# Kernel optimization log

Measured on AMD Instinct MI355X. Metric: run time of the kernel, lower is better.

## Reference

```python
import jax, jax.numpy as jnp
import numpy as np

N_NODES = 200000
N_EDGES = 6400000
N_GRAPHS = 128


def setup_inputs() -> dict:
    key = jax.random.key(0)
    k1, k2, k3, k4, k5, k6, k7 = jax.random.split(key, 7)
    x = jax.random.normal(k1, (N_NODES, 1), dtype=jnp.float32)
    edge_index = jax.random.randint(k2, (2, N_EDGES), 0, N_NODES, dtype=jnp.int64)
    batch = jnp.sort(jax.random.randint(k3, (N_NODES,), 0, N_GRAPHS, dtype=jnp.int64))
    # GCNConv parameters (glorot-ish scale)
    W1 = jax.random.normal(k4, (1, 32), dtype=jnp.float32) * (1.0 / np.sqrt(1 + 32))
    b1 = jnp.zeros((32,), dtype=jnp.float32)
    W2 = jax.random.normal(k5, (32, 8), dtype=jnp.float32) * (1.0 / np.sqrt(32 + 8))
    b2 = jnp.zeros((8,), dtype=jnp.float32)
    return {"x": x, "edge_index": edge_index, "batch": batch,
            "W1": W1, "b1": b1, "W2": W2, "b2": b2}


def _gcn_conv(x, src, dst, W, b):
    # x: [N, din] -> [N, dout]; PyG GCNConv: symmetric-normalized A+I aggregation
    h = x @ W                                            # [N, dout]
    deg = jax.ops.segment_sum(jnp.ones_like(dst, h.dtype), dst, num_segments=N_NODES)
    dinv = jnp.where(deg > 0, jax.lax.rsqrt(deg), 0.0)    # [N]
    norm = dinv[src] * dinv[dst]                          # [E+N]
    msg = h[src] * norm[:, None]                          # gather + scale
    out = jax.ops.segment_sum(msg, dst, num_segments=N_NODES)
    return out + b


def reference(x, edge_index, batch, W1, b1, W2, b2):
    loop = jnp.arange(N_NODES, dtype=edge_index.dtype)
    src = jnp.concatenate([edge_index[0], loop])          # add self-loops
    dst = jnp.concatenate([edge_index[1], loop])
    h = _gcn_conv(x, src, dst, W1, b1)
    h = _gcn_conv(h, src, dst, W2, b2)
    # global mean pool over graphs
    sums = jax.ops.segment_sum(h, batch, num_segments=N_GRAPHS)
    cnts = jax.ops.segment_sum(jnp.ones((N_NODES,), h.dtype), batch, num_segments=N_GRAPHS)
    pooled = sums / jnp.maximum(cnts, 1.0)[:, None]       # [G, 8]
    return jax.nn.log_softmax(pooled, axis=1)
```

## Files before the change

### kernel.cpp

```cpp
#include <hip/hip_runtime.h>
#include <math.h>

#define N_NODES 200000
#define N_EDGES 6400000
#define N_GRAPHS 128

#define NBK   782
#define EBLK  256
#define EPB   (N_EDGES / EBLK)


__global__ void kA0_hist(const int* __restrict__ dst, unsigned* __restrict__ countMat) {
    __shared__ unsigned cnt[NBK];
    for (int t = threadIdx.x; t < NBK; t += blockDim.x) cnt[t] = 0;
    __syncthreads();
    const int4* d4 = (const int4*)(dst + blockIdx.x * EPB);
    for (int e = threadIdx.x; e < EPB / 4; e += blockDim.x) {
        int4 d = d4[e];
        atomicAdd(&cnt[d.x >> 8], 1u);
        atomicAdd(&cnt[d.y >> 8], 1u);
        atomicAdd(&cnt[d.z >> 8], 1u);
        atomicAdd(&cnt[d.w >> 8], 1u);
    }
    __syncthreads();
    for (int t = threadIdx.x; t < NBK; t += blockDim.x)
        countMat[blockIdx.x * NBK + t] = cnt[t];
}

__global__ void kScanBlk(unsigned* __restrict__ mat, unsigned* __restrict__ colsum) {
    int bkt = blockIdx.x * 4 + (threadIdx.x >> 6);
    if (bkt >= NBK) return;
    int lane = threadIdx.x & 63;
    unsigned carry = 0;
    for (int k = 0; k < 4; ++k) {
        int blk = k * 64 + lane;
        unsigned v = mat[blk * NBK + bkt];
        unsigned s = v;
        for (int off = 1; off < 64; off <<= 1) {
            unsigned u = __shfl_up(s, off);
            if (lane >= off) s += u;
        }
        mat[blk * NBK + bkt] = carry + s - v;
        carry += __shfl(s, 63);
    }
    colsum[bkt] = carry;
}

__global__ void kScanBkt(const unsigned* __restrict__ colsum, unsigned* __restrict__ bucketBase) {
    __shared__ unsigned wsum[16];
    int t = threadIdx.x;
    int lane = t & 63, w = t >> 6;
    unsigned v = (t < NBK) ? colsum[t] : 0u;
    unsigned s = v;
    for (int off = 1; off < 64; off <<= 1) {
        unsigned u = __shfl_up(s, off);
        if (lane >= off) s += u;
    }
    if (lane == 63) wsum[w] = s;
    __syncthreads();
    if (w == 0 && lane < 16) {
        int nw = blockDim.x >> 6;
        unsigned ws = (lane < nw) ? wsum[lane] : 0u;
        unsigned ss = ws;
        for (int off = 1; off < 16; off <<= 1) {
            unsigned u = __shfl_up(ss, off);
            if (lane >= off) ss += u;
        }
        wsum[lane] = ss - ws;
    }
    __syncthreads();
    unsigned excl = s - v + wsum[w];
    if (t < NBK) bucketBase[t] = excl;
    if (t == NBK - 1) bucketBase[NBK] = excl + v;
}

__global__ void kA1_scatter(const int* __restrict__ src, const int* __restrict__ dst,
                            const unsigned* __restrict__ baseMat,
                            const unsigned* __restrict__ bucketBase,
                            unsigned* __restrict__ binned) {
    __shared__ unsigned cur[NBK];
    for (int t = threadIdx.x; t < NBK; t += blockDim.x)
        cur[t] = baseMat[blockIdx.x * NBK + t] + bucketBase[t];
    __syncthreads();
    const int base_e = blockIdx.x * EPB;
    const int4* s4 = (const int4*)(src + base_e);
    const int4* d4 = (const int4*)(dst + base_e);
    for (int e = threadIdx.x; e < EPB / 4; e += blockDim.x) {
        int4 s = s4[e];
        int4 d = d4[e];
        unsigned p;
        p = atomicAdd(&cur[d.x >> 8], 1u); binned[p] = ((unsigned)s.x << 8) | (unsigned)(d.x & 255);
        p = atomicAdd(&cur[d.y >> 8], 1u); binned[p] = ((unsigned)s.y << 8) | (unsigned)(d.y & 255);
        p = atomicAdd(&cur[d.z >> 8], 1u); binned[p] = ((unsigned)s.z << 8) | (unsigned)(d.z & 255);
        p = atomicAdd(&cur[d.w >> 8], 1u); binned[p] = ((unsigned)s.w << 8) | (unsigned)(d.w & 255);
    }
}

__global__ void __launch_bounds__(512)
kB_deg(const unsigned* __restrict__ binned, const unsigned* __restrict__ bucketBase,
       const float* __restrict__ x, float* __restrict__ dinv, float* __restrict__ xd) {
    __shared__ unsigned deg[256];
    if (threadIdx.x < 256) deg[threadIdx.x] = 0;
    __syncthreads();
    int b = blockIdx.x;
    unsigned lo = bucketBase[b], hi = bucketBase[b + 1];
    const uint4* b4 = (const uint4*)binned;
    for (unsigned q = lo / 4 + threadIdx.x; q * 4 < hi; q += blockDim.x) {
        uint4 v = b4[q];
        unsigned e0 = q * 4;
        if (e0 >= lo && e0 + 3 < hi) {
            atomicAdd(&deg[v.x & 255u], 1u);
            atomicAdd(&deg[v.y & 255u], 1u);
            atomicAdd(&deg[v.z & 255u], 1u);
            atomicAdd(&deg[v.w & 255u], 1u);
        } else {
            if (e0     >= lo && e0     < hi) atomicAdd(&deg[v.x & 255u], 1u);
            if (e0 + 1 >= lo && e0 + 1 < hi) atomicAdd(&deg[v.y & 255u], 1u);
            if (e0 + 2 >= lo && e0 + 2 < hi) atomicAdd(&deg[v.z & 255u], 1u);
            if (e0 + 3 >= lo && e0 + 3 < hi) atomicAdd(&deg[v.w & 255u], 1u);
        }
    }
    __syncthreads();
    if (threadIdx.x < 256) {
        int node = b * 256 + threadIdx.x;
        if (node < N_NODES) {
            float di = rsqrtf((float)deg[threadIdx.x] + 1.0f);
            dinv[node] = di;
            xd[node] = x[node] * di;
        }
    }
}

__global__ void __launch_bounds__(512)
kC_pass1(const unsigned* __restrict__ binned, const unsigned* __restrict__ bucketBase,
         const float* __restrict__ xd, const float* __restrict__ dinv,
         float2* __restrict__ pair) {
    __shared__ float tacc[256];
    if (threadIdx.x < 256) tacc[threadIdx.x] = 0.0f;
    __syncthreads();
    int b = blockIdx.x;
    unsigned lo = bucketBase[b], hi = bucketBase[b + 1];
    const uint4* b4 = (const uint4*)binned;
    for (unsigned q = lo / 4 + threadIdx.x; q * 4 < hi; q += blockDim.x) {
        uint4 v = b4[q];
        unsigned e0 = q * 4;
        float g0 = xd[v.x >> 8];
        float g1 = xd[v.y >> 8];
        float g2 = xd[v.z >> 8];
        float g3 = xd[v.w >> 8];
        if (e0 >= lo && e0 + 3 < hi) {
            atomicAdd(&tacc[v.x & 255u], g0);
            atomicAdd(&tacc[v.y & 255u], g1);
            atomicAdd(&tacc[v.z & 255u], g2);
            atomicAdd(&tacc[v.w & 255u], g3);
        } else {
            if (e0     >= lo && e0     < hi) atomicAdd(&tacc[v.x & 255u], g0);
            if (e0 + 1 >= lo && e0 + 1 < hi) atomicAdd(&tacc[v.y & 255u], g1);
            if (e0 + 2 >= lo && e0 + 2 < hi) atomicAdd(&tacc[v.z & 255u], g2);
            if (e0 + 3 >= lo && e0 + 3 < hi) atomicAdd(&tacc[v.w & 255u], g3);
        }
    }
    __syncthreads();
    if (threadIdx.x < 256) {
        int node = b * 256 + threadIdx.x;
        if (node < N_NODES) {
            float di = dinv[node];
            float a = di * (tacc[threadIdx.x] + xd[node]);
            pair[node] = make_float2(a * di, di);
        }
    }
}

__global__ void __launch_bounds__(512)
kD_pass2(const unsigned* __restrict__ binned, const unsigned* __restrict__ bucketBase,
         const float2* __restrict__ pair, const int* __restrict__ batch,
         float* __restrict__ gacc) {
    __shared__ float s1a[256], s0a[256];
    if (threadIdx.x < 256) { s1a[threadIdx.x] = 0.0f; s0a[threadIdx.x] = 0.0f; }
    __syncthreads();
    int b = blockIdx.x;
    unsigned lo = bucketBase[b], hi = bucketBase[b + 1];
    const uint4* b4 = (const uint4*)binned;
    for (unsigned q = lo / 4 + threadIdx.x; q * 4 < hi; q += blockDim.x) {
        uint4 v = b4[q];
        unsigned e0 = q * 4;
        float2 p0 = pair[v.x >> 8];
        float2 p1 = pair[v.y >> 8];
        float2 p2 = pair[v.z >> 8];
        float2 p3 = pair[v.w >> 8];
        if (e0 >= lo && e0 + 3 < hi) {
            atomicAdd(&s1a[v.x & 255u], p0.x); atomicAdd(&s0a[v.x & 255u], p0.y);
            atomicAdd(&s1a[v.y & 255u], p1.x); atomicAdd(&s0a[v.y & 255u], p1.y);
            atomicAdd(&s1a[v.z & 255u], p2.x); atomicAdd(&s0a[v.z & 255u], p2.y);
            atomicAdd(&s1a[v.w & 255u], p3.x); atomicAdd(&s0a[v.w & 255u], p3.y);
        } else {
            if (e0     >= lo && e0     < hi) { atomicAdd(&s1a[v.x & 255u], p0.x); atomicAdd(&s0a[v.x & 255u], p0.y); }
            if (e0 + 1 >= lo && e0 + 1 < hi) { atomicAdd(&s1a[v.y & 255u], p1.x); atomicAdd(&s0a[v.y & 255u], p1.y); }
            if (e0 + 2 >= lo && e0 + 2 < hi) { atomicAdd(&s1a[v.z & 255u], p2.x); atomicAdd(&s0a[v.z & 255u], p2.y); }
            if (e0 + 3 >= lo && e0 + 3 < hi) { atomicAdd(&s1a[v.w & 255u], p3.x); atomicAdd(&s0a[v.w & 255u], p3.y); }
        }
    }
    __syncthreads();
    if (threadIdx.x < 256) {
        int node = b * 256 + threadIdx.x;
        float s1f = 0.0f, s0f = 0.0f;
        int g = 0;
        bool valid = (node < N_NODES);
        if (valid) {
            float2 pr = pair[node];
            float di = pr.y;
            s1f = di * (s1a[threadIdx.x] + pr.x);
            s0f = di * (s0a[threadIdx.x] + di);
            g = batch[node];
        }
        int g0 = __shfl(g, 0);
        bool uni = __all(valid && (g == g0));
        if (uni) {
            for (int off = 32; off; off >>= 1) {
                s1f += __shfl_down(s1f, off);
                s0f += __shfl_down(s0f, off);
            }
            if ((threadIdx.x & 63) == 0) {
                atomicAdd(&gacc[g0], s1f);
                atomicAdd(&gacc[N_GRAPHS + g0], s0f);
                atomicAdd(&gacc[2 * N_GRAPHS + g0], 64.0f);
            }
        } else if (valid) {
            atomicAdd(&gacc[g], s1f);
            atomicAdd(&gacc[N_GRAPHS + g], s0f);
            atomicAdd(&gacc[2 * N_GRAPHS + g], 1.0f);
        }
    }
}

__global__ void k_final(const float* __restrict__ gacc,
                        const float* __restrict__ W1, const float* __restrict__ b1,
                        const float* __restrict__ W2, const float* __restrict__ b2,
                        float* __restrict__ out) {
    int g = threadIdx.x;
    if (g >= N_GRAPHS) return;
    float GS1 = gacc[g];
    float GS0 = gacc[N_GRAPHS + g];
    float cnt = gacc[2 * N_GRAPHS + g];
    float denom = fmaxf(cnt, 1.0f);
    float p[8];
    for (int k = 0; k < 8; ++k) {
        float u = 0.0f, v = 0.0f;
        for (int c = 0; c < 32; ++c) {
            u += W1[c] * W2[c * 8 + k];
            v += b1[c] * W2[c * 8 + k];
        }
        p[k] = (u * GS1 + v * GS0 + cnt * b2[k]) / denom;
    }
    float m = p[0];
    for (int k = 1; k < 8; ++k) m = fmaxf(m, p[k]);
    float s = 0.0f;
    for (int k = 0; k < 8; ++k) s += expf(p[k] - m);
    float l = logf(s);
    for (int k = 0; k < 8; ++k) out[g * 8 + k] = p[k] - m - l;
}


__global__ void k_deg(const int* __restrict__ dst, float* __restrict__ deg) {
    const int4* d4 = (const int4*)dst;
    const int n4 = N_EDGES / 4;
    for (int e = blockIdx.x * blockDim.x + threadIdx.x; e < n4; e += gridDim.x * blockDim.x) {
        int4 d = d4[e];
        atomicAdd(&deg[d.x], 1.0f);
        atomicAdd(&deg[d.y], 1.0f);
        atomicAdd(&deg[d.z], 1.0f);
        atomicAdd(&deg[d.w], 1.0f);
    }
}

__global__ void k_dinv(const float* __restrict__ x, float* __restrict__ deg_dinv,
                       float* __restrict__ xd) {
    int i = blockIdx.x * blockDim.x + threadIdx.x;
    if (i < N_NODES) {
        float dinv = rsqrtf(deg_dinv[i] + 1.0f);
        deg_dinv[i] = dinv;
        xd[i] = x[i] * dinv;
    }
}

__global__ void k_pass1(const int* __restrict__ src, const int* __restrict__ dst,
                        const float* __restrict__ xd, float* __restrict__ t) {
    const int4* s4 = (const int4*)src;
    const int4* d4 = (const int4*)dst;
    const int n4 = N_EDGES / 4;
    for (int e = blockIdx.x * blockDim.x + threadIdx.x; e < n4; e += gridDim.x * blockDim.x) {
        int4 s = s4[e];
        int4 d = d4[e];
        atomicAdd(&t[d.x], xd[s.x]);
        atomicAdd(&t[d.y], xd[s.y]);
        atomicAdd(&t[d.z], xd[s.z]);
        atomicAdd(&t[d.w], xd[s.w]);
    }
}

__global__ void k_agg1(const float* __restrict__ dinv, const float* __restrict__ xd,
                       float* __restrict__ t, float2* __restrict__ pair) {
    int i = blockIdx.x * blockDim.x + threadIdx.x;
    if (i < N_NODES) {
        float di = dinv[i];
        float a = di * (t[i] + xd[i]);
        t[i] = a;
        pair[i] = make_float2(a * di, di);
    }
}

__global__ void k_pass2(const int* __restrict__ src, const int* __restrict__ dst,
                        const float2* __restrict__ pair,
                        float* __restrict__ s1, float* __restrict__ s0) {
    const int4* s4 = (const int4*)src;
    const int4* d4 = (const int4*)dst;
    const int n4 = N_EDGES / 4;
    for (int e = blockIdx.x * blockDim.x + threadIdx.x; e < n4; e += gridDim.x * blockDim.x) {
        int4 s = s4[e];
        int4 d = d4[e];
        float2 p0 = pair[s.x];
        float2 p1 = pair[s.y];
        float2 p2 = pair[s.z];
        float2 p3 = pair[s.w];
        atomicAdd(&s1[d.x], p0.x); atomicAdd(&s0[d.x], p0.y);
        atomicAdd(&s1[d.y], p1.x); atomicAdd(&s0[d.y], p1.y);
        atomicAdd(&s1[d.z], p2.x); atomicAdd(&s0[d.z], p2.y);
        atomicAdd(&s1[d.w], p3.x); atomicAdd(&s0[d.w], p3.y);
    }
}

__global__ void k_node2(const float* __restrict__ dinv, const float* __restrict__ agg1,
                        const float* __restrict__ s1, const float* __restrict__ s0,
                        const int* __restrict__ batch, float* __restrict__ gacc) {
    int i = blockIdx.x * blockDim.x + threadIdx.x;
    float s1f = 0.0f, s0f = 0.0f;
    int g = 0;
    bool valid = (i < N_NODES);
    if (valid) {
        float di = dinv[i];
        s1f = di * (s1[i] + agg1[i] * di);
        s0f = di * (s0[i] + di);
        g = batch[i];
    }
    int g0 = __shfl(g, 0);
    bool uni = __all(valid && (g == g0));
    if (uni) {
        for (int off = 32; off; off >>= 1) {
            s1f += __shfl_down(s1f, off);
            s0f += __shfl_down(s0f, off);
        }
        if ((threadIdx.x & 63) == 0) {
            atomicAdd(&gacc[g0], s1f);
            atomicAdd(&gacc[N_GRAPHS + g0], s0f);
            atomicAdd(&gacc[2 * N_GRAPHS + g0], 64.0f);
        }
    } else if (valid) {
        atomicAdd(&gacc[g], s1f);
        atomicAdd(&gacc[N_GRAPHS + g], s0f);
        atomicAdd(&gacc[2 * N_GRAPHS + g], 1.0f);
    }
}


extern "C" void kernel_launch(void* const* d_in, const int* in_sizes, int n_in,
                              void* d_out, int out_size, void* d_ws, size_t ws_size,
                              hipStream_t stream) {
    const float* x     = (const float*)d_in[0];
    const int*   edge  = (const int*)d_in[1];
    const int*   batch = (const int*)d_in[2];
    const float* W1    = (const float*)d_in[3];
    const float* b1    = (const float*)d_in[4];
    const float* W2    = (const float*)d_in[5];
    const float* b2    = (const float*)d_in[6];
    float* out = (float*)d_out;

    const int* src = edge;
    const int* dst = edge + N_EDGES;

    const size_t o_binned = 0;
    const size_t o_cmat   = o_binned + (size_t)N_EDGES;
    const size_t o_colsum = o_cmat + (size_t)EBLK * NBK;
    const size_t o_bbase  = o_colsum + NBK;
    const size_t o_dinv   = o_bbase + NBK + 1;
    const size_t o_xd     = o_dinv + N_NODES;
    size_t o_pair         = o_xd + N_NODES;
    if (o_pair & 1) o_pair++;
    const size_t o_gacc   = o_pair + 2 * (size_t)N_NODES;
    const size_t need_u32 = o_gacc + 3 * N_GRAPHS;

    unsigned* ws_u = (unsigned*)d_ws;
    float*    ws_f = (float*)d_ws;

    if (ws_size >= need_u32 * 4) {
        unsigned* binned     = ws_u + o_binned;
        unsigned* countMat   = ws_u + o_cmat;
        unsigned* colsum     = ws_u + o_colsum;
        unsigned* bucketBase = ws_u + o_bbase;
        float*    dinv       = ws_f + o_dinv;
        float*    xd         = ws_f + o_xd;
        float2*   pair       = (float2*)(ws_f + o_pair);
        float*    gacc       = ws_f + o_gacc;

        hipMemsetAsync(gacc, 0, 3 * N_GRAPHS * sizeof(float), stream);

        kA0_hist   <<<EBLK, 256, 0, stream>>>(dst, countMat);
        kScanBlk   <<<(NBK + 3) / 4, 256, 0, stream>>>(countMat, colsum);
        kScanBkt   <<<1, 832, 0, stream>>>(colsum, bucketBase);
        kA1_scatter<<<EBLK, 256, 0, stream>>>(src, dst, countMat, bucketBase, binned);
        kB_deg     <<<NBK, 512, 0, stream>>>(binned, bucketBase, x, dinv, xd);
        kC_pass1   <<<NBK, 512, 0, stream>>>(binned, bucketBase, xd, dinv, pair);
        kD_pass2   <<<NBK, 512, 0, stream>>>(binned, bucketBase, pair, batch, gacc);
        k_final    <<<1, 128, 0, stream>>>(gacc, W1, b1, W2, b2, out);
    } else {
        float* dinv = ws_f;
        float* t    = ws_f + 1 * N_NODES;
        float* s1   = ws_f + 2 * N_NODES;
        float* s0   = ws_f + 3 * N_NODES;
        float* xd   = ws_f + 4 * N_NODES;
        float2* pair = (float2*)(ws_f + 5 * N_NODES);
        float* gacc = ws_f + 7 * N_NODES;

        hipMemsetAsync(ws_f, 0, (size_t)4 * N_NODES * sizeof(float), stream);
        hipMemsetAsync(gacc, 0, (size_t)3 * N_GRAPHS * sizeof(float), stream);

        const int EB = 2048, ET = 256;
        const int NB = (N_NODES + 255) / 256, NT = 256;

        k_deg  <<<EB, ET, 0, stream>>>(dst, dinv);
        k_dinv <<<NB, NT, 0, stream>>>(x, dinv, xd);
        k_pass1<<<EB, ET, 0, stream>>>(src, dst, xd, t);
        k_agg1 <<<NB, NT, 0, stream>>>(dinv, xd, t, pair);
        k_pass2<<<EB, ET, 0, stream>>>(src, dst, pair, s1, s0);
        k_node2<<<NB, NT, 0, stream>>>(dinv, t, s1, s0, batch, gacc);
        k_final<<<1, 128, 0, stream>>>(gacc, W1, b1, W2, b2, out);
    }
}
```

Baseline: 229.6 us.

## Use 196-node buckets, more edge blocks, and prefetch binned loads in passes

Shrinks the destination bucket size from 256 to 196 nodes, so there are 1021 buckets and more gather/accumulate blocks, and raises the edge-partition block count from 256 to 2000 to spread the histogram and scatter phases over more workgroups. The scan kernels are generalised to the larger block count, and the count matrix is padded to 1024 columns. The two aggregation passes software-prefetch the next uint4 of binned edges before processing the current one. The costs are a division per edge for the bucket index, a larger count matrix to scan, and kScanBkt now assuming NBK fits in 1024 threads with 16 wave sums.

```diff
diff --git a/kernel.cpp b/kernel.cpp
--- a/kernel.cpp
+++ b/kernel.cpp
@@ -5,9 +5,13 @@
 #define N_EDGES 6400000
 #define N_GRAPHS 128
 
-#define NBK   782
-#define EBLK  256
+#define BSZ   196
+#define NBK   1021
+#define NBKP  1024
+#define EBLK  2000
 #define EPB   (N_EDGES / EBLK)
+
+static __device__ __forceinline__ unsigned bkt_of(unsigned node) { return node / (unsigned)BSZ; }
 
 
 __global__ void kA0_hist(const int* __restrict__ dst, unsigned* __restrict__ countMat) {
@@ -17,14 +21,14 @@
     const int4* d4 = (const int4*)(dst + blockIdx.x * EPB);
     for (int e = threadIdx.x; e < EPB / 4; e += blockDim.x) {
         int4 d = d4[e];
-        atomicAdd(&cnt[d.x >> 8], 1u);
-        atomicAdd(&cnt[d.y >> 8], 1u);
-        atomicAdd(&cnt[d.z >> 8], 1u);
-        atomicAdd(&cnt[d.w >> 8], 1u);
+        atomicAdd(&cnt[bkt_of((unsigned)d.x)], 1u);
+        atomicAdd(&cnt[bkt_of((unsigned)d.y)], 1u);
+        atomicAdd(&cnt[bkt_of((unsigned)d.z)], 1u);
+        atomicAdd(&cnt[bkt_of((unsigned)d.w)], 1u);
     }
     __syncthreads();
     for (int t = threadIdx.x; t < NBK; t += blockDim.x)
-        countMat[blockIdx.x * NBK + t] = cnt[t];
+        countMat[blockIdx.x * NBKP + t] = cnt[t];
 }
 
 __global__ void kScanBlk(unsigned* __restrict__ mat, unsigned* __restrict__ colsum) {
@@ -32,15 +36,16 @@
     if (bkt >= NBK) return;
     int lane = threadIdx.x & 63;
     unsigned carry = 0;
-    for (int k = 0; k < 4; ++k) {
+    const int rounds = (EBLK + 63) / 64;
+    for (int k = 0; k < rounds; ++k) {
         int blk = k * 64 + lane;
-        unsigned v = mat[blk * NBK + bkt];
+        unsigned v = (blk < EBLK) ? mat[blk * NBKP + bkt] : 0u;
         unsigned s = v;
         for (int off = 1; off < 64; off <<= 1) {
             unsigned u = __shfl_up(s, off);
             if (lane >= off) s += u;
         }
-        mat[blk * NBK + bkt] = carry + s - v;
+        if (blk < EBLK) mat[blk * NBKP + bkt] = carry + s - v;
         carry += __shfl(s, 63);
     }
     colsum[bkt] = carry;
@@ -80,7 +85,7 @@
                             unsigned* __restrict__ binned) {
     __shared__ unsigned cur[NBK];
     for (int t = threadIdx.x; t < NBK; t += blockDim.x)
-        cur[t] = baseMat[blockIdx.x * NBK + t] + bucketBase[t];
+        cur[t] = baseMat[blockIdx.x * NBKP + t] + bucketBase[t];
     __syncthreads();
     const int base_e = blockIdx.x * EPB;
     const int4* s4 = (const int4*)(src + base_e);
@@ -88,19 +93,23 @@
     for (int e = threadIdx.x; e < EPB / 4; e += blockDim.x) {
         int4 s = s4[e];
         int4 d = d4[e];
+        unsigned b0 = bkt_of((unsigned)d.x), l0 = (unsigned)d.x - b0 * BSZ;
+        unsigned b1 = bkt_of((unsigned)d.y), l1 = (unsigned)d.y - b1 * BSZ;
+        unsigned b2 = bkt_of((unsigned)d.z), l2 = (unsigned)d.z - b2 * BSZ;
+        unsigned b3 = bkt_of((unsigned)d.w), l3 = (unsigned)d.w - b3 * BSZ;
         unsigned p;
-        p = atomicAdd(&cur[d.x >> 8], 1u); binned[p] = ((unsigned)s.x << 8) | (unsigned)(d.x & 255);
-        p = atomicAdd(&cur[d.y >> 8], 1u); binned[p] = ((unsigned)s.y << 8) | (unsigned)(d.y & 255);
-        p = atomicAdd(&cur[d.z >> 8], 1u); binned[p] = ((unsigned)s.z << 8) | (unsigned)(d.z & 255);
-        p = atomicAdd(&cur[d.w >> 8], 1u); binned[p] = ((unsigned)s.w << 8) | (unsigned)(d.w & 255);
+        p = atomicAdd(&cur[b0], 1u); binned[p] = ((unsigned)s.x << 8) | l0;
+        p = atomicAdd(&cur[b1], 1u); binned[p] = ((unsigned)s.y << 8) | l1;
+        p = atomicAdd(&cur[b2], 1u); binned[p] = ((unsigned)s.z << 8) | l2;
+        p = atomicAdd(&cur[b3], 1u); binned[p] = ((unsigned)s.w << 8) | l3;
     }
 }
 
 __global__ void __launch_bounds__(512)
 kB_deg(const unsigned* __restrict__ binned, const unsigned* __restrict__ bucketBase,
        const float* __restrict__ x, float* __restrict__ dinv, float* __restrict__ xd) {
-    __shared__ unsigned deg[256];
-    if (threadIdx.x < 256) deg[threadIdx.x] = 0;
+    __shared__ unsigned deg[BSZ];
+    if (threadIdx.x < BSZ) deg[threadIdx.x] = 0;
     __syncthreads();
     int b = blockIdx.x;
     unsigned lo = bucketBase[b], hi = bucketBase[b + 1];
@@ -121,8 +130,8 @@
         }
     }
     __syncthreads();
-    if (threadIdx.x < 256) {
-        int node = b * 256 + threadIdx.x;
+    if (threadIdx.x < BSZ) {
+        int node = b * BSZ + threadIdx.x;
         if (node < N_NODES) {
             float di = rsqrtf((float)deg[threadIdx.x] + 1.0f);
             dinv[node] = di;
@@ -135,19 +144,25 @@
 kC_pass1(const unsigned* __restrict__ binned, const unsigned* __restrict__ bucketBase,
          const float* __restrict__ xd, const float* __restrict__ dinv,
          float2* __restrict__ pair) {
-    __shared__ float tacc[256];
-    if (threadIdx.x < 256) tacc[threadIdx.x] = 0.0f;
+    __shared__ float tacc[BSZ];
+    if (threadIdx.x < BSZ) tacc[threadIdx.x] = 0.0f;
     __syncthreads();
     int b = blockIdx.x;
     unsigned lo = bucketBase[b], hi = bucketBase[b + 1];
     const uint4* b4 = (const uint4*)binned;
-    for (unsigned q = lo / 4 + threadIdx.x; q * 4 < hi; q += blockDim.x) {
-        uint4 v = b4[q];
-        unsigned e0 = q * 4;
+
+    unsigned q = lo / 4 + threadIdx.x;
+    bool act = (q * 4 < hi);
+    uint4 v = act ? b4[q] : make_uint4(0, 0, 0, 0);
+    while (act) {
+        unsigned qn = q + blockDim.x;
+        bool actn = (qn * 4 < hi);
+        uint4 vn = actn ? b4[qn] : v;
         float g0 = xd[v.x >> 8];
         float g1 = xd[v.y >> 8];
         float g2 = xd[v.z >> 8];
         float g3 = xd[v.w >> 8];
+        unsigned e0 = q * 4;
         if (e0 >= lo && e0 + 3 < hi) {
             atomicAdd(&tacc[v.x & 255u], g0);
             atomicAdd(&tacc[v.y & 255u], g1);
@@ -159,10 +174,11 @@
             if (e0 + 2 >= lo && e0 + 2 < hi) atomicAdd(&tacc[v.z & 255u], g2);
             if (e0 + 3 >= lo && e0 + 3 < hi) atomicAdd(&tacc[v.w & 255u], g3);
         }
-    }
-    __syncthreads();
-    if (threadIdx.x < 256) {
-        int node = b * 256 + threadIdx.x;
+        q = qn; act = actn; v = vn;
+    }
+    __syncthreads();
+    if (threadIdx.x < BSZ) {
+        int node = b * BSZ + threadIdx.x;
         if (node < N_NODES) {
             float di = dinv[node];
             float a = di * (tacc[threadIdx.x] + xd[node]);
@@ -175,19 +191,25 @@
 kD_pass2(const unsigned* __restrict__ binned, const unsigned* __restrict__ bucketBase,
          const float2* __restrict__ pair, const int* __restrict__ batch,
          float* __restrict__ gacc) {
-    __shared__ float s1a[256], s0a[256];
-    if (threadIdx.x < 256) { s1a[threadIdx.x] = 0.0f; s0a[threadIdx.x] = 0.0f; }
+    __shared__ float s1a[BSZ], s0a[BSZ];
+    if (threadIdx.x < BSZ) { s1a[threadIdx.x] = 0.0f; s0a[threadIdx.x] = 0.0f; }
     __syncthreads();
     int b = blockIdx.x;
     unsigned lo = bucketBase[b], hi = bucketBase[b + 1];
     const uint4* b4 = (const uint4*)binned;
-    for (unsigned q = lo / 4 + threadIdx.x; q * 4 < hi; q += blockDim.x) {
-        uint4 v = b4[q];
-        unsigned e0 = q * 4;
+
+    unsigned q = lo / 4 + threadIdx.x;
+    bool act = (q * 4 < hi);
+    uint4 v = act ? b4[q] : make_uint4(0, 0, 0, 0);
+    while (act) {
+        unsigned qn = q + blockDim.x;
+        bool actn = (qn * 4 < hi);
+        uint4 vn = actn ? b4[qn] : v;
         float2 p0 = pair[v.x >> 8];
         float2 p1 = pair[v.y >> 8];
         float2 p2 = pair[v.z >> 8];
         float2 p3 = pair[v.w >> 8];
+        unsigned e0 = q * 4;
         if (e0 >= lo && e0 + 3 < hi) {
             atomicAdd(&s1a[v.x & 255u], p0.x); atomicAdd(&s0a[v.x & 255u], p0.y);
             atomicAdd(&s1a[v.y & 255u], p1.x); atomicAdd(&s0a[v.y & 255u], p1.y);
@@ -199,13 +221,14 @@
             if (e0 + 2 >= lo && e0 + 2 < hi) { atomicAdd(&s1a[v.z & 255u], p2.x); atomicAdd(&s0a[v.z & 255u], p2.y); }
             if (e0 + 3 >= lo && e0 + 3 < hi) { atomicAdd(&s1a[v.w & 255u], p3.x); atomicAdd(&s0a[v.w & 255u], p3.y); }
         }
+        q = qn; act = actn; v = vn;
     }
     __syncthreads();
     if (threadIdx.x < 256) {
-        int node = b * 256 + threadIdx.x;
+        int node = b * BSZ + threadIdx.x;
         float s1f = 0.0f, s0f = 0.0f;
         int g = 0;
-        bool valid = (node < N_NODES);
+        bool valid = (threadIdx.x < BSZ) && (node < N_NODES);
         if (valid) {
             float2 pr = pair[node];
             float di = pr.y;
@@ -379,9 +402,9 @@
 
     const size_t o_binned = 0;
     const size_t o_cmat   = o_binned + (size_t)N_EDGES;
-    const size_t o_colsum = o_cmat + (size_t)EBLK * NBK;
-    const size_t o_bbase  = o_colsum + NBK;
-    const size_t o_dinv   = o_bbase + NBK + 1;
+    const size_t o_colsum = o_cmat + (size_t)EBLK * NBKP;
+    const size_t o_bbase  = o_colsum + NBKP;
+    const size_t o_dinv   = o_bbase + NBKP;
     const size_t o_xd     = o_dinv + N_NODES;
     size_t o_pair         = o_xd + N_NODES;
     if (o_pair & 1) o_pair++;
@@ -405,7 +428,7 @@
 
         kA0_hist   <<<EBLK, 256, 0, stream>>>(dst, countMat);
         kScanBlk   <<<(NBK + 3) / 4, 256, 0, stream>>>(countMat, colsum);
-        kScanBkt   <<<1, 832, 0, stream>>>(colsum, bucketBase);
+        kScanBkt   <<<1, 1024, 0, stream>>>(colsum, bucketBase);
         kA1_scatter<<<EBLK, 256, 0, stream>>>(src, dst, countMat, bucketBase, binned);
         kB_deg     <<<NBK, 512, 0, stream>>>(binned, bucketBase, x, dinv, xd);
         kC_pass1   <<<NBK, 512, 0, stream>>>(binned, bucketBase, xd, dinv, pair);
```

Result: slower. 271.9 us (+18.4%).
